# Kernel tuning notes

Measured on AMD Instinct MI355X. Metric: run time of the kernel, lower is better.

Reference implementation:

```python
import jax, jax.numpy as jnp
import numpy as np

P = 10      # qubits
LQ = 4      # re-uploading layers
B = 4096    # batch
HID = 32    # readout hidden
DIM = 2 ** P


def _rz(t):
    t = jnp.asarray(t, jnp.float32)
    e = jnp.exp(-0.5j * t.astype(jnp.complex64))
    z = jnp.zeros_like(e)
    return jnp.stack([jnp.stack([e, z], -1), jnp.stack([z, jnp.conj(e)], -1)], -2)


def _rx(t):
    t = jnp.asarray(t, jnp.float32)
    c = jnp.cos(0.5 * t).astype(jnp.complex64)
    s = jnp.sin(0.5 * t).astype(jnp.complex64)
    return jnp.stack([jnp.stack([c, -1j * s], -1), jnp.stack([-1j * s, c], -1)], -2)


def _ry(t):
    t = jnp.asarray(t, jnp.float32)
    c = jnp.cos(0.5 * t).astype(jnp.complex64)
    s = jnp.sin(0.5 * t).astype(jnp.complex64)
    return jnp.stack([jnp.stack([c, -s], -1), jnp.stack([s, c], -1)], -2)


def _apply_1q(state, U, k):
    # state [B, 2^P] complex, U [B,2,2]; wire 0 = most-significant bit (PennyLane order)
    b = state.shape[0]
    s = state.reshape(b, 2 ** k, 2, -1)
    s = jnp.einsum('bij,bajc->baic', U, s)
    return s.reshape(b, -1)


def _apply_cnot(state, c, t):
    b = state.shape[0]
    a, d = min(c, t), max(c, t)
    s = state.reshape(b, 2 ** a, 2, 2 ** (d - a - 1), 2, -1)
    if c == a:  # control = smaller wire index (axis 2), target at axis 4
        hi = jnp.flip(s[:, :, 1], axis=3)  # [b,pre,mid,2,post] -> flip target bit
        s = jnp.stack([s[:, :, 0], hi], axis=2)
    else:       # control = larger wire index (axis 4), target at axis 2
        hi = jnp.flip(s[:, :, :, :, 1], axis=2)  # [b,pre,2,mid,post] -> flip target bit
        s = jnp.stack([s[:, :, :, :, 0], hi], axis=4)
    return s.reshape(b, -1)


def _meas_signs(p):
    # rows 0..p-1: Z_k signs; rows p..2p-1: Z_k Z_{(k+1)%p} signs
    idx = np.arange(2 ** p)
    bits = (idx[None, :] >> (p - 1 - np.arange(p)[:, None])) & 1
    z = (1.0 - 2.0 * bits).astype(np.float32)            # [p, 2^p]
    zz = z * np.roll(z, -1, axis=0)                      # [p, 2^p]
    return jnp.asarray(np.concatenate([z, zz], axis=0))  # [2p, 2^p]


MEAS = _meas_signs(P)


def _circuit_feats(theta, rot_weights, enc_scale, enc_bias):
    b = theta.shape[0]
    # Hadamard on every wire of |0...0> -> uniform superposition
    state = jnp.full((b, DIM), 1.0 / np.sqrt(DIM), dtype=jnp.complex64)
    for l in range(LQ):
        for k in range(P):
            t0 = enc_scale[l, k, 0] * theta[:, k] + enc_bias[l, k, 0]
            t1 = enc_scale[l, k, 1] * theta[:, k] + enc_bias[l, k, 1]
            U_enc = jnp.einsum('bij,bjk->bik', _rx(t1), _rz(t0))  # RX(t1) RZ(t0)
            w = rot_weights[l, k]
            # PennyLane Rot(phi,theta,omega) = RZ(omega) RY(theta) RZ(phi)
            U_rot = _rz(w[2]) @ _ry(w[1]) @ _rz(w[0])
            U = jnp.einsum('ij,bjk->bik', U_rot, U_enc)
            state = _apply_1q(state, U, k)
        for k in range(P):
            state = _apply_cnot(state, k, (k + 1) % P)
    probs = jnp.abs(state) ** 2              # [B, 2^P]
    return probs @ MEAS.T                    # [B, 2P] expectation values


def setup_inputs() -> dict:
    key = jax.random.key(0)
    ks = jax.random.split(key, 4)
    theta = jax.random.uniform(ks[0], (B, P), jnp.float32, -np.pi, np.pi)
    rot_weights = 0.02 * jax.random.normal(ks[1], (LQ, P, 3), dtype=jnp.float32)
    enc_scale = jnp.ones((LQ, P, 2), jnp.float32)   # clamp(0.5,1.5) of ones = ones
    enc_bias = jnp.zeros((LQ, P, 2), jnp.float32)
    n_meas = 2 * P
    W1 = jax.random.normal(ks[2], (HID, n_meas), dtype=jnp.float32) / np.sqrt(n_meas)
    b1 = jnp.zeros((HID,), jnp.float32)
    W2 = jax.random.normal(ks[3], (1, HID), dtype=jnp.float32) / np.sqrt(HID)
    b2 = jnp.zeros((1,), jnp.float32)
    return dict(theta=theta, rot_weights=rot_weights, enc_scale=enc_scale,
                enc_bias=enc_bias, W1=W1, b1=b1, W2=W2, b2=b2)


def reference(theta, rot_weights, enc_scale, enc_bias, W1, b1, W2, b2):
    feats = _circuit_feats(theta, rot_weights, enc_scale, enc_bias)
    h = jax.nn.silu(feats @ W1.T + b1)
    return (h @ W2.T + b2)[:, 0]  # [B]
```

## Files before the change

kernel.cpp:

```cpp
#include <hip/hip_runtime.h>
#include <math.h>

#define NQ   10
#define NLAY 4
#define BATCH 4096
#define HID  32
#define NM   20

typedef float    f2  __attribute__((ext_vector_type(2)));
typedef unsigned u2v __attribute__((ext_vector_type(2)));

struct Tables {
    unsigned col[NLAY + 1][NQ];
    unsigned row[NLAY + 1][NQ];
};

constexpr Tables make_tables() {
    Tables t{};
    unsigned col[NQ] = {}, row[NQ] = {};
    for (int k = 0; k < NQ; ++k) { col[k] = 1u << (NQ - 1 - k); row[k] = 1u << (NQ - 1 - k); }
    for (int l = 0; l <= NLAY; ++l) {
        for (int k = 0; k < NQ; ++k) { t.col[l][k] = col[k]; t.row[l][k] = row[k]; }
        for (int k = 0; k < NQ; ++k) {
            int c = k, tg = (k + 1) % NQ;
            col[c] ^= col[tg];
            row[tg] ^= row[c];
        }
    }
    return t;
}

static constexpr Tables TB = make_tables();

struct cpx { float x, y; };
__device__ __forceinline__ cpx cxmul(cpx a, cpx b) {
    return { fmaf(a.x, b.x, -a.y * b.y), fmaf(a.x, b.y, a.y * b.x) };
}

__device__ __forceinline__ f2 mk2(float a, float b) { f2 r; r[0] = a; r[1] = b; return r; }
__device__ __forceinline__ f2 ffma(f2 a, f2 b, f2 c) { return __builtin_elementwise_fma(a, b, c); }

__device__ __forceinline__ f2 cmac(f2 acc, f2 a, f2 b) {
    acc = ffma(mk2(a[0], a[0]), b, acc);
    acc = ffma(mk2(-a[1], a[1]), mk2(b[1], b[0]), acc);
    return acc;
}

template<int CTRL>
__device__ __forceinline__ float dppf(float x) {
    return __int_as_float(__builtin_amdgcn_update_dpp(
        0, __float_as_int(x), CTRL, 0xF, 0xF, true));
}

template<unsigned M>
__device__ __forceinline__ float dpplo(float x) {
    static_assert(M < 16u, "dpplo handles masks 0..15");
    if constexpr (M == 0u)       return x;
    else if constexpr (M == 1u)  return dppf<0xB1>(x);
    else if constexpr (M == 2u)  return dppf<0x4E>(x);
    else if constexpr (M == 3u)  return dppf<0x1B>(x);
    else if constexpr (M == 7u)  return dppf<0x141>(x);
    else if constexpr (M == 8u)  return dppf<0x128>(x);
    else if constexpr (M == 15u) return dppf<0x140>(x);
    else if constexpr (M == 4u)  return dppf<0x141>(dppf<0x1B>(x));
    else if constexpr (M == 5u)  return dppf<0x141>(dppf<0x4E>(x));
    else if constexpr (M == 6u)  return dppf<0x141>(dppf<0xB1>(x));
    else if constexpr (M == 9u)  return dppf<0x128>(dppf<0xB1>(x));
    else if constexpr (M == 10u) return dppf<0x128>(dppf<0x4E>(x));
    else if constexpr (M == 11u) return dppf<0x128>(dppf<0x1B>(x));
    else if constexpr (M == 12u) return dppf<0x140>(dppf<0x1B>(x));
    else if constexpr (M == 13u) return dppf<0x140>(dppf<0x4E>(x));
    else                         return dppf<0x140>(dppf<0xB1>(x));
}

__device__ __forceinline__ float redfold16(float x) {
#if __has_builtin(__builtin_amdgcn_permlane16_swap)
    u2v r = __builtin_amdgcn_permlane16_swap(__float_as_uint(x), __float_as_uint(x), false, false);
    return __uint_as_float(r[0]) + __uint_as_float(r[1]);
#else
    return x + __shfl_xor(x, 16);
#endif
}

template<unsigned M>
__device__ __forceinline__ float xlane(float x) {
    if constexpr (M == 0u) return x;
    else if constexpr ((M & 16u) != 0u)
        return __int_as_float(__builtin_amdgcn_ds_swizzle(
            __float_as_int(x), (int)((M << 10) | 0x1F)));
    else return dpplo<M>(x);
}

template<int L, int K>
__device__ __forceinline__ void apply_gate(f2 (&st)[32], const float4 (*gm)[2],
                                           const int lane) {
    constexpr unsigned v     = TB.col[L][K];
    constexpr unsigned m     = TB.row[L][K];
    constexpr unsigned vlane = (v >> 5) & 31u;
    constexpr int      vr    = (int)(v & 31u);
    constexpr unsigned mlane = (m >> 5) & 31u;
    constexpr int      mr    = (int)(m & 31u);
    constexpr int      gi    = L * NQ + K;

    int laneP = 0;
    if constexpr (mlane != 0u) laneP = __popc((unsigned)lane & mlane) & 1;
    const float4 A = gm[gi][laneP];
    const f2 ocA = mk2(A.x, A.y), pcA = mk2(A.z, A.w);
    f2 ocB = ocA, pcB = pcA;
    if constexpr (mr != 0) {
        const float4 B = gm[gi][laneP ^ 1];
        ocB = mk2(B.x, B.y); pcB = mk2(B.z, B.w);
    }

    #pragma unroll
    for (int r = 0; r < 32; ++r) {
        const int r2 = r ^ vr;
        if (r2 < r) continue;
        f2 p_r, p_r2;
        if constexpr (vlane != 0u) {
            p_r = mk2(xlane<vlane>(st[r2][0]), xlane<vlane>(st[r2][1]));
            if (r2 != r)
                p_r2 = mk2(xlane<vlane>(st[r][0]), xlane<vlane>(st[r][1]));
        } else {
            p_r = st[r2];
            p_r2 = st[r];
        }
        {
            const int pr = __builtin_popcount((unsigned)(r & mr)) & 1;
            const f2 oc = pr ? ocB : ocA;
            const f2 pc = pr ? pcB : pcA;
            f2 acc = mk2(0.f, 0.f);
            acc = cmac(acc, oc, st[r]);
            acc = cmac(acc, pc, p_r);
            if (r2 != r) {
                const int pr2 = __builtin_popcount((unsigned)(r2 & mr)) & 1;
                const f2 oc2 = pr2 ? ocB : ocA;
                const f2 pc2 = pr2 ? pcB : pcA;
                f2 acc2 = mk2(0.f, 0.f);
                acc2 = cmac(acc2, oc2, st[r2]);
                acc2 = cmac(acc2, pc2, p_r2);
                st[r2] = acc2;
            }
            st[r] = acc;
        }
    }
}

__global__ __launch_bounds__(256, 2)
void qrh_kernel(
    const float* __restrict__ theta, const float* __restrict__ rotw,
    const float* __restrict__ escale, const float* __restrict__ ebias,
    const float* __restrict__ W1, const float* __restrict__ b1,
    const float* __restrict__ W2, const float* __restrict__ b2,
    float* __restrict__ out)
{
    __shared__ float4 gmat[8 * NLAY * NQ][2];
    __shared__ float4 wtab[8][NQ];

    const int tid  = threadIdx.x;
    const int lane = tid & 63;
    const int wv   = tid >> 6;
    const int e    = (wv << 1) | (lane >> 5);
    const int b    = blockIdx.x * 8 + e;

    for (int g = tid; g < 8 * NLAY * NQ; g += 256) {
        const int ge = g / (NLAY * NQ);
        const int gg = g % (NLAY * NQ);
        const int l = gg / NQ, k = gg % NQ;
        const int gb = blockIdx.x * 8 + ge;
        const float th = theta[gb * NQ + k];
        const int e2 = (l * NQ + k) * 2;
        const float t0 = escale[e2 + 0] * th + ebias[e2 + 0];
        const float t1 = escale[e2 + 1] * th + ebias[e2 + 1];
        float sn0, c0, sn1, c1;
        __sincosf(0.5f * t0, &sn0, &c0);
        __sincosf(0.5f * t1, &sn1, &c1);
        const f2 E00 = mk2( c1 * c0,  -c1 * sn0);
        const f2 E01 = mk2( sn1 * sn0, -sn1 * c0);
        const f2 E10 = mk2(-sn1 * sn0, -sn1 * c0);
        const f2 E11 = mk2( c1 * c0,   c1 * sn0);
        const int r3 = (l * NQ + k) * 3;
        const float w0 = rotw[r3 + 0], w1 = rotw[r3 + 1], w2 = rotw[r3 + 2];
        float cw, sw, ca0, sa0, ca1, sa1;
        __sincosf(0.5f * w1, &sw, &cw);
        __sincosf(0.5f * (w0 + w2), &sa0, &ca0);
        __sincosf(0.5f * (w0 - w2), &sa1, &ca1);
        const f2 R00 = mk2( cw * ca0, -cw * sa0);
        const f2 R01 = mk2(-sw * ca1, -sw * sa1);
        const f2 R10 = mk2( sw * ca1, -sw * sa1);
        const f2 R11 = mk2( cw * ca0,  cw * sa0);
        auto cm = [](f2 a, f2 bb) { return mk2(a[0]*bb[0] - a[1]*bb[1], a[0]*bb[1] + a[1]*bb[0]); };
        const f2 U00 = cm(R00, E00) + cm(R01, E10);
        const f2 U01 = cm(R00, E01) + cm(R01, E11);
        const f2 U10 = cm(R10, E00) + cm(R11, E10);
        const f2 U11 = cm(R10, E01) + cm(R11, E11);
        gmat[g][0] = make_float4(U00[0], U00[1], U01[0], U01[1]);
        gmat[g][1] = make_float4(U11[0], U11[1], U10[0], U10[1]);
        if (l == 0) {
            const float inv = 0.70710678118654752f;
            const f2 al = (U00 + U01) * inv;
            const f2 be = (U10 + U11) * inv;
            wtab[ge][k] = make_float4(al[0], al[1], be[0], be[1]);
        }
    }
    __syncthreads();

    if (wv & 1) { __builtin_amdgcn_s_sleep(10); __builtin_amdgcn_s_sleep(10); }

    const int hl = lane & 31;
    f2 st[32];
    {
        cpx pre;
        {
            const float4 q = wtab[e][0];
            pre = ((hl >> 4) & 1) ? cpx{q.z, q.w} : cpx{q.x, q.y};
            #pragma unroll
            for (int k = 1; k < 5; ++k) {
                const float4 t = wtab[e][k];
                const cpx w_ = ((hl >> (4 - k)) & 1) ? cpx{t.z, t.w} : cpx{t.x, t.y};
                pre = cxmul(pre, w_);
            }
        }
        const float4 q5 = wtab[e][5], q6 = wtab[e][6], q7 = wtab[e][7];
        const float4 q8 = wtab[e][8], q9 = wtab[e][9];
        const cpx w5[2] = {{q5.x, q5.y}, {q5.z, q5.w}};
        const cpx w6[2] = {{q6.x, q6.y}, {q6.z, q6.w}};
        const cpx w7[2] = {{q7.x, q7.y}, {q7.z, q7.w}};
        const cpx w8[2] = {{q8.x, q8.y}, {q8.z, q8.w}};
        const cpx w9[2] = {{q9.x, q9.y}, {q9.z, q9.w}};
        cpx a7[8];
        #pragma unroll
        for (int j = 0; j < 8; ++j)
            a7[j] = cxmul(cxmul(cxmul(pre, w5[j >> 2]), w6[(j >> 1) & 1]), w7[j & 1]);
        #pragma unroll
        for (int r = 0; r < 32; ++r) {
            const cpx t = cxmul(cxmul(a7[r >> 2], w8[(r >> 1) & 1]), w9[r & 1]);
            st[r] = mk2(t.x, t.y);
        }
    }

    const float4 (*gm)[2] = &gmat[e * NLAY * NQ];

    #define GATE(L,K) apply_gate<L,K>(st, gm, lane);
    #define LAYER(L) GATE(L,0) GATE(L,1) GATE(L,2) GATE(L,3) GATE(L,4) \
                     GATE(L,5) GATE(L,6) GATE(L,7) GATE(L,8) GATE(L,9)
    LAYER(1)
    LAYER(2)
    LAYER(3)
    #undef LAYER
    #undef GATE

    float w[32];
    #pragma unroll
    for (int r = 0; r < 32; ++r) {
        const f2 sq = st[r] * st[r];
        w[r] = sq[0] + sq[1];
    }
    #pragma unroll
    for (int bit = 1; bit < 32; bit <<= 1) {
        #pragma unroll
        for (int j = 0; j < 32; ++j) {
            if (!(j & bit)) {
                const float a = w[j], c = w[j | bit];
                w[j] = a + c; w[j | bit] = a - c;
            }
        }
    }

    float feats[NM];
    #pragma unroll
    for (int f = 0; f < NM; ++f) {
        const unsigned M = (f < NQ) ? TB.row[NLAY][f]
                                    : (TB.row[NLAY][f - NQ] ^ TB.row[NLAY][(f - NQ + 1) % NQ]);
        const unsigned Mlane = (M >> 5) & 31u;
        const int Mr = (int)(M & 31u);
        const float s = w[Mr];
        const int lsgn = __popc((unsigned)lane & Mlane) & 1;
        feats[f] = lsgn ? -s : s;
    }
    #pragma unroll
    for (int f = 0; f < NM; ++f) {
        float v = feats[f];
        v += dppf<0xB1>(v);
        v += dppf<0x4E>(v);
        v += dppf<0x141>(v);
        v += dppf<0x128>(v);
        v = redfold16(v);
        feats[f] = v;
    }

    float part;
    {
        float acc = b1[hl];
        #pragma unroll
        for (int mm = 0; mm < NM; ++mm) acc = fmaf(feats[mm], W1[hl * NM + mm], acc);
        const float sg = 1.f / (1.f + __expf(-acc));
        part = acc * sg * W2[hl];
    }
    part += dppf<0xB1>(part);
    part += dppf<0x4E>(part);
    part += dppf<0x141>(part);
    part += dppf<0x128>(part);
    part = redfold16(part);
    if (hl == 0) out[b] = part + b2[0];
}

extern "C" void kernel_launch(void* const* d_in, const int* in_sizes, int n_in,
                              void* d_out, int out_size, void* d_ws, size_t ws_size,
                              hipStream_t stream) {
    (void)in_sizes; (void)n_in; (void)out_size; (void)d_ws; (void)ws_size;
    const float* theta = (const float*)d_in[0];
    const float* rotw  = (const float*)d_in[1];
    const float* esc   = (const float*)d_in[2];
    const float* ebi   = (const float*)d_in[3];
    const float* W1    = (const float*)d_in[4];
    const float* b1    = (const float*)d_in[5];
    const float* W2    = (const float*)d_in[6];
    const float* b2    = (const float*)d_in[7];
    float* out = (float*)d_out;

    qrh_kernel<<<BATCH / 8, 256, 0, stream>>>(theta, rotw, esc, ebi, W1, b1, W2, b2, out);
}
```

Baseline: 91.49 us.

## Spread each sample's statevector over a full 64-lane wave with 16 amplitudes per lane

Each batch element now occupies a whole wavefront instead of half of one, so each lane holds 16 complex amplitudes instead of 32. Gates acting on the top lane bit use __shfl_xor (ds_bpermute), and the reductions gain a permlane32 fold. Blocks now hold 4 samples and the launch bound rises to 4 blocks per CU, aiming to cut register pressure and raise occupancy. The cost is more cross-lane traffic, duplicated readout MLP work (corrected by a 0.5 factor), and the half-1 waves now doing the shared-memory gate setup work for half as many samples per block.

```diff
diff --git a/kernel.cpp b/kernel.cpp
--- a/kernel.cpp
+++ b/kernel.cpp
@@ -82,9 +82,20 @@
 #endif
 }
 
+__device__ __forceinline__ float redfold32(float x) {
+#if __has_builtin(__builtin_amdgcn_permlane32_swap)
+    u2v r = __builtin_amdgcn_permlane32_swap(__float_as_uint(x), __float_as_uint(x), false, false);
+    return __uint_as_float(r[0]) + __uint_as_float(r[1]);
+#else
+    return x + __shfl_xor(x, 32);
+#endif
+}
+
 template<unsigned M>
 __device__ __forceinline__ float xlane(float x) {
     if constexpr (M == 0u) return x;
+    else if constexpr ((M & 32u) != 0u)
+        return __shfl_xor(x, (int)M);
     else if constexpr ((M & 16u) != 0u)
         return __int_as_float(__builtin_amdgcn_ds_swizzle(
             __float_as_int(x), (int)((M << 10) | 0x1F)));
@@ -92,14 +103,14 @@
 }
 
 template<int L, int K>
-__device__ __forceinline__ void apply_gate(f2 (&st)[32], const float4 (*gm)[2],
+__device__ __forceinline__ void apply_gate(f2 (&st)[16], const float4 (*gm)[2],
                                            const int lane) {
     constexpr unsigned v     = TB.col[L][K];
     constexpr unsigned m     = TB.row[L][K];
-    constexpr unsigned vlane = (v >> 5) & 31u;
-    constexpr int      vr    = (int)(v & 31u);
-    constexpr unsigned mlane = (m >> 5) & 31u;
-    constexpr int      mr    = (int)(m & 31u);
+    constexpr unsigned vlane = (v >> 4) & 63u;
+    constexpr int      vr    = (int)(v & 15u);
+    constexpr unsigned mlane = (m >> 4) & 63u;
+    constexpr int      mr    = (int)(m & 15u);
     constexpr int      gi    = L * NQ + K;
 
     int laneP = 0;
@@ -113,7 +124,7 @@
     }
 
     #pragma unroll
-    for (int r = 0; r < 32; ++r) {
+    for (int r = 0; r < 16; ++r) {
         const int r2 = r ^ vr;
         if (r2 < r) continue;
         f2 p_r, p_r2;
@@ -146,7 +157,7 @@
     }
 }
 
-__global__ __launch_bounds__(256, 2)
+__global__ __launch_bounds__(256, 4)
 void qrh_kernel(
     const float* __restrict__ theta, const float* __restrict__ rotw,
     const float* __restrict__ escale, const float* __restrict__ ebias,
@@ -154,20 +165,20 @@
     const float* __restrict__ W2, const float* __restrict__ b2,
     float* __restrict__ out)
 {
-    __shared__ float4 gmat[8 * NLAY * NQ][2];
-    __shared__ float4 wtab[8][NQ];
+    __shared__ float4 gmat[4 * NLAY * NQ][2];
+    __shared__ float4 wtab[4][NQ];
 
     const int tid  = threadIdx.x;
     const int lane = tid & 63;
     const int wv   = tid >> 6;
-    const int e    = (wv << 1) | (lane >> 5);
-    const int b    = blockIdx.x * 8 + e;
-
-    for (int g = tid; g < 8 * NLAY * NQ; g += 256) {
+    const int e    = wv;
+    const int b    = blockIdx.x * 4 + e;
+
+    for (int g = tid; g < 4 * NLAY * NQ; g += 256) {
         const int ge = g / (NLAY * NQ);
         const int gg = g % (NLAY * NQ);
         const int l = gg / NQ, k = gg % NQ;
-        const int gb = blockIdx.x * 8 + ge;
+        const int gb = blockIdx.x * 4 + ge;
         const float th = theta[gb * NQ + k];
         const int e2 = (l * NQ + k) * 2;
         const float t0 = escale[e2 + 0] * th + ebias[e2 + 0];
@@ -207,34 +218,36 @@
 
     if (wv & 1) { __builtin_amdgcn_s_sleep(10); __builtin_amdgcn_s_sleep(10); }
 
-    const int hl = lane & 31;
-    f2 st[32];
+    f2 st[16];
     {
         cpx pre;
         {
             const float4 q = wtab[e][0];
-            pre = ((hl >> 4) & 1) ? cpx{q.z, q.w} : cpx{q.x, q.y};
+            pre = ((lane >> 5) & 1) ? cpx{q.z, q.w} : cpx{q.x, q.y};
             #pragma unroll
-            for (int k = 1; k < 5; ++k) {
+            for (int k = 1; k < 6; ++k) {
                 const float4 t = wtab[e][k];
-                const cpx w_ = ((hl >> (4 - k)) & 1) ? cpx{t.z, t.w} : cpx{t.x, t.y};
+                const cpx w_ = ((lane >> (5 - k)) & 1) ? cpx{t.z, t.w} : cpx{t.x, t.y};
                 pre = cxmul(pre, w_);
             }
         }
-        const float4 q5 = wtab[e][5], q6 = wtab[e][6], q7 = wtab[e][7];
+        const float4 q6 = wtab[e][6], q7 = wtab[e][7];
         const float4 q8 = wtab[e][8], q9 = wtab[e][9];
-        const cpx w5[2] = {{q5.x, q5.y}, {q5.z, q5.w}};
         const cpx w6[2] = {{q6.x, q6.y}, {q6.z, q6.w}};
         const cpx w7[2] = {{q7.x, q7.y}, {q7.z, q7.w}};
         const cpx w8[2] = {{q8.x, q8.y}, {q8.z, q8.w}};
         const cpx w9[2] = {{q9.x, q9.y}, {q9.z, q9.w}};
-        cpx a7[8];
-        #pragma unroll
-        for (int j = 0; j < 8; ++j)
-            a7[j] = cxmul(cxmul(cxmul(pre, w5[j >> 2]), w6[(j >> 1) & 1]), w7[j & 1]);
-        #pragma unroll
-        for (int r = 0; r < 32; ++r) {
-            const cpx t = cxmul(cxmul(a7[r >> 2], w8[(r >> 1) & 1]), w9[r & 1]);
+        cpx a67[4];
+        #pragma unroll
+        for (int j = 0; j < 4; ++j)
+            a67[j] = cxmul(cxmul(pre, w6[j >> 1]), w7[j & 1]);
+        cpx w89[4];
+        #pragma unroll
+        for (int j = 0; j < 4; ++j)
+            w89[j] = cxmul(w8[j >> 1], w9[j & 1]);
+        #pragma unroll
+        for (int r = 0; r < 16; ++r) {
+            const cpx t = cxmul(a67[r >> 2], w89[r & 3]);
             st[r] = mk2(t.x, t.y);
         }
     }
@@ -250,16 +263,16 @@
     #undef LAYER
     #undef GATE
 
-    float w[32];
-    #pragma unroll
-    for (int r = 0; r < 32; ++r) {
+    float w[16];
+    #pragma unroll
+    for (int r = 0; r < 16; ++r) {
         const f2 sq = st[r] * st[r];
         w[r] = sq[0] + sq[1];
     }
     #pragma unroll
-    for (int bit = 1; bit < 32; bit <<= 1) {
-        #pragma unroll
-        for (int j = 0; j < 32; ++j) {
+    for (int bit = 1; bit < 16; bit <<= 1) {
+        #pragma unroll
+        for (int j = 0; j < 16; ++j) {
             if (!(j & bit)) {
                 const float a = w[j], c = w[j | bit];
                 w[j] = a + c; w[j | bit] = a - c;
@@ -272,8 +285,8 @@
     for (int f = 0; f < NM; ++f) {
         const unsigned M = (f < NQ) ? TB.row[NLAY][f]
                                     : (TB.row[NLAY][f - NQ] ^ TB.row[NLAY][(f - NQ + 1) % NQ]);
-        const unsigned Mlane = (M >> 5) & 31u;
-        const int Mr = (int)(M & 31u);
+        const unsigned Mlane = (M >> 4) & 63u;
+        const int Mr = (int)(M & 15u);
         const float s = w[Mr];
         const int lsgn = __popc((unsigned)lane & Mlane) & 1;
         feats[f] = lsgn ? -s : s;
@@ -286,9 +299,11 @@
         v += dppf<0x141>(v);
         v += dppf<0x128>(v);
         v = redfold16(v);
+        v = redfold32(v);
         feats[f] = v;
     }
 
+    const int hl = lane & 31;
     float part;
     {
         float acc = b1[hl];
@@ -302,7 +317,8 @@
     part += dppf<0x141>(part);
     part += dppf<0x128>(part);
     part = redfold16(part);
-    if (hl == 0) out[b] = part + b2[0];
+    part = redfold32(part);
+    if (lane == 0) out[b] = fmaf(0.5f, part, b2[0]);
 }
 
 extern "C" void kernel_launch(void* const* d_in, const int* in_sizes, int n_in,
@@ -319,5 +335,5 @@
     const float* b2    = (const float*)d_in[7];
     float* out = (float*)d_out;
 
-    qrh_kernel<<<BATCH / 8, 256, 0, stream>>>(theta, rotw, esc, ebi, W1, b1, W2, b2, out);
-}
+    qrh_kernel<<<BATCH / 4, 256, 0, stream>>>(theta, rotw, esc, ebi, W1, b1, W2, b2, out);
+}
```

New measurement: 97.08 us. 1.06x slower.
